# Performance work log

Measured on AMD Instinct MI355X. Metric: run time of the kernel, lower is better.

The kernel has to match this reference:

```python
import jax, jax.numpy as jnp
import numpy as np

EPS = 1e-5


def _gcn_conv(x, src, dst, norm, W, b, n_nodes):
    # PyG GCNConv: transform, then normalized scatter-add aggregation (self-loops included in src/dst)
    h = x @ W                                   # [N, out]
    msg = h[src] * norm[:, None]                # gather over edges [E+N, out]
    agg = jax.ops.segment_sum(msg, dst, num_segments=n_nodes)
    return agg + b


def _bn(x, gamma, beta):
    # BatchNorm1d in training mode: batch stats over node axis, biased variance
    mu = jnp.mean(x, axis=0)
    var = jnp.mean((x - mu) ** 2, axis=0)
    return (x - mu) * jax.lax.rsqrt(var + EPS) * gamma + beta


def setup_inputs() -> dict:
    key = jax.random.key(0)
    ks = jax.random.split(key, 8)
    N, E, F_in, H, F_out = 50000, 800000, 32, 96, 2
    x = jax.random.normal(ks[0], (N, F_in), dtype=jnp.float32)
    edge_index = jax.random.randint(ks[1], (2, E), 0, N, dtype=jnp.int64)
    def lin(k, fi, fo):
        s = 1.0 / np.sqrt(fi)
        return jax.random.uniform(k, (fi, fo), jnp.float32, -s, s)
    W1 = lin(ks[2], F_in, H); b1 = jnp.zeros((H,), jnp.float32)
    W2 = lin(ks[3], H, H);    b2 = jnp.zeros((H,), jnp.float32)
    W3 = lin(ks[4], H, H);    b3 = jnp.zeros((H,), jnp.float32)
    W4 = lin(ks[5], H, F_out); b4 = jnp.zeros((F_out,), jnp.float32)
    g1 = jnp.ones((H,), jnp.float32); be1 = jnp.zeros((H,), jnp.float32)
    g2 = jnp.ones((H,), jnp.float32); be2 = jnp.zeros((H,), jnp.float32)
    g3 = jnp.ones((H,), jnp.float32); be3 = jnp.zeros((H,), jnp.float32)
    return dict(x=x, edge_index=edge_index,
                W1=W1, b1=b1, g1=g1, be1=be1,
                W2=W2, b2=b2, g2=g2, be2=be2,
                W3=W3, b3=b3, g3=g3, be3=be3,
                W4=W4, b4=b4)


def reference(x, edge_index, W1, b1, g1, be1, W2, b2, g2, be2, W3, b3, g3, be3, W4, b4):
    N = x.shape[0]
    loop = jnp.arange(N, dtype=edge_index.dtype)
    src = jnp.concatenate([edge_index[0], loop])   # add self-loops
    dst = jnp.concatenate([edge_index[1], loop])
    deg = jax.ops.segment_sum(jnp.ones_like(dst, dtype=x.dtype), dst, num_segments=N)
    dinv = jnp.where(deg > 0, jax.lax.rsqrt(deg), 0.0)
    norm = dinv[src] * dinv[dst]                   # D^{-1/2} (A+I) D^{-1/2}

    h = jax.nn.relu(_bn(_gcn_conv(x, src, dst, norm, W1, b1, N), g1, be1))
    h = jax.nn.relu(_bn(_gcn_conv(h, src, dst, norm, W2, b2, N), g2, be2))
    h = jax.nn.relu(_bn(_gcn_conv(h, src, dst, norm, W3, b3, N), g3, be3))
    return _gcn_conv(h, src, dst, norm, W4, b4, N)
```

## Files before the change

kernel.cpp:

```cpp
#include <hip/hip_runtime.h>
#include <hip/hip_bf16.h>

using bf16x8 = __attribute__((ext_vector_type(8))) short;
using f32x4  = __attribute__((ext_vector_type(4))) float;

#define FS_CHUNK 4096

__device__ __forceinline__ float ldf(const void* p, size_t i, float isf){
  if (isf > 0.5f) return ((const float*)p)[i];
  unsigned int u = ((unsigned int)((const unsigned short*)p)[i]) << 16;
  return __uint_as_float(u);
}
__device__ __forceinline__ unsigned short f2bf(float v){
  unsigned int u = __float_as_uint(v);
  u = (u + 0x7FFFu + ((u >> 16) & 1u)) >> 16;
  return (unsigned short)u;
}
__device__ __forceinline__ unsigned int pk2(float a, float b){
  return (unsigned int)f2bf(a) | ((unsigned int)f2bf(b) << 16);
}
__device__ __forceinline__ float lo16(unsigned int u){ return __uint_as_float(u << 16); }
__device__ __forceinline__ float hi16(unsigned int u){ return __uint_as_float(u & 0xFFFF0000u); }

__global__ void k_fill(unsigned short* o, unsigned short v, int n){
  int i = blockIdx.x*blockDim.x + threadIdx.x;
  if (i < n) o[i] = v;
}

__global__ void k_prep(const unsigned short* xh, const unsigned int* eu,
                       float* flag, int nelemX, long long E,
                       const void* W1, const void* W2, const void* W3, const void* W4,
                       unsigned short* __restrict__ Wt1, unsigned short* __restrict__ Wt2,
                       unsigned short* __restrict__ Wt3, float* __restrict__ W4f,
                       int* __restrict__ cnt, float* __restrict__ stAll, int n){
  int t = threadIdx.x;
  if (blockIdx.x > 0){
    int total = n + 4609;
    for (int i = (int)(blockIdx.x-1)*256 + t; i < total; i += (int)(gridDim.x-1)*256){
      if (i < n) cnt[i] = 0; else stAll[i - n] = 0.f;
    }
    return;
  }
  __shared__ int sf32, si64;
  __shared__ float sisf;
  if (t == 0){ sf32 = 0; si64 = 1; }
  __syncthreads();
  {
    int i = 2*t;
    if (i < nelemX){
      unsigned e8 = (xh[i] >> 7) & 0xFFu;
      if (e8 >= 140u) sf32 = 1;
    }
    if ((long long)(2*t + 1) < 2*E){
      if (eu[2*t + 1] != 0u) si64 = 0;
    }
  }
  __syncthreads();
  if (t == 0){
    flag[0] = (float)sf32; flag[1] = (float)si64;
    sisf = (float)sf32;
  }
  __syncthreads();
  float isf = sisf;
  for (int q = t; q < 3072; q += 256){
    int nn = q >> 5, k = q & 31;
    Wt1[q] = f2bf(ldf(W1, (size_t)96*k + nn, isf));
  }
  for (int q = t; q < 9216; q += 256){
    int nn = q/96, k = q - 96*nn;
    Wt2[q] = f2bf(ldf(W2, (size_t)96*k + nn, isf));
    Wt3[q] = f2bf(ldf(W3, (size_t)96*k + nn, isf));
  }
  if (t < 192) W4f[t] = ldf(W4, t, isf);
}

__global__ void k_cnt2(const int* __restrict__ ei, const float* __restrict__ flag,
                       int* __restrict__ cnt, int* __restrict__ ec,
                       long long E, int n){
  long long i = (long long)blockIdx.x*blockDim.x + threadIdx.x;
  long long i0 = 2*i;
  if (i0 >= E) return;
  bool i64 = (flag[1] > 0.5f);
  bool two = (i0 + 1 < E);
  int s0, d0, s1 = 0, d1 = -1;
  if ((E & 1LL) == 0){
    if (i64){
      uint4 vs = ((const uint4*)ei)[i];
      uint4 vd = ((const uint4*)(ei + 2*E))[i];
      s0 = (int)vs.x; s1 = (int)vs.z; d0 = (int)vd.x; d1 = (int)vd.z;
    } else {
      int2 vs = ((const int2*)ei)[i];
      int2 vd = ((const int2*)(ei + E))[i];
      s0 = vs.x; s1 = vs.y; d0 = vd.x; d1 = vd.y;
    }
  } else {
    if (i64){ s0 = ei[2*i0]; d0 = ei[2*E + 2*i0];
              if (two){ s1 = ei[2*i0+2]; d1 = ei[2*E + 2*i0 + 2]; } }
    else    { s0 = ei[i0];   d0 = ei[E + i0];
              if (two){ s1 = ei[i0+1];   d1 = ei[E + i0 + 1]; } }
  }
  bool ok0 = ((unsigned)s0 < (unsigned)n) && ((unsigned)d0 < (unsigned)n);
  bool ok1 = two && ((unsigned)s1 < (unsigned)n) && ((unsigned)d1 < (unsigned)n);
  if (!ok0){ s0 = -1; d0 = -1; }
  if (!ok1){ s1 = -1; d1 = -1; }
  if (two){
    int4 o; o.x = s0; o.y = d0; o.z = s1; o.w = d1;
    ((int4*)ec)[i] = o;
  } else {
    int2 o; o.x = s0; o.y = d0;
    ((int2*)ec)[i0] = o;
  }
  if (ok0) atomicAdd(&cnt[d0], 1);
  if (ok1) atomicAdd(&cnt[d1], 1);
}

__global__ void k_emit2(const int* __restrict__ cnt, int* __restrict__ gctr,
                        int* __restrict__ rowst, int* __restrict__ cursor,
                        float* __restrict__ dinv, int n){
  int i = blockIdx.x*256 + threadIdx.x;
  int lane = threadIdx.x & 63;
  int v = (i < n) ? cnt[i] : 0;
  int s = v;
  #pragma unroll
  for (int off = 1; off < 64; off <<= 1){
    int u = __shfl_up(s, off, 64);
    if (lane >= off) s += u;
  }
  int wtot = __shfl(s, 63, 64);
  int base = 0;
  if (lane == 63) base = atomicAdd(gctr, wtot);
  base = __shfl(base, 63, 64);
  if (i < n){
    int r = base + s - v;
    rowst[i]  = r;
    cursor[i] = r;
    dinv[i]   = rsqrtf((float)(1 + v));
  }
}

template<typename IT>
__global__ __launch_bounds__(256) void k_fx(const int* __restrict__ ec,
      int* __restrict__ cursor, IT* __restrict__ csr,
      long long E, int n, int gF8,
      const void* __restrict__ x, const float* __restrict__ flag,
      const float* __restrict__ dinv, unsigned short* __restrict__ XS){
  int t = threadIdx.x;
  if ((int)blockIdx.x < gF8){
    int part = blockIdx.x & 7;
    long long base = (long long)(blockIdx.x >> 3) * FS_CHUNK;
    int pl = (int)(((long long)n *  part     ) >> 3);
    int pr = (int)(((long long)n * (part + 1)) >> 3);
    long long lim = base + FS_CHUNK < E ? base + FS_CHUNK : E;
    for (long long i = base + 2*t; i < lim; i += 512){
      int4 v = ((const int4*)ec)[i >> 1];
      if (v.y >= pl && v.y < pr && (unsigned)v.x < (unsigned)n){
        int p = atomicAdd(&cursor[v.y], 1);
        csr[p] = (IT)v.x;
      }
      if (i + 1 < lim && v.w >= pl && v.w < pr && (unsigned)v.z < (unsigned)n){
        int p = atomicAdd(&cursor[v.w], 1);
        csr[p] = (IT)v.z;
      }
    }
    return;
  }
  int q = (int)(blockIdx.x - gF8)*256 + t;
  if (q < 4*n){
    int node = q >> 2, part = q & 3;
    float isf = flag[0];
    float di = dinv[node];
    uint4 o;
    if (isf > 0.5f){
      const float* xr = (const float*)x + (size_t)32*node + 8*part;
      o.x = pk2(xr[0]*di, xr[1]*di); o.y = pk2(xr[2]*di, xr[3]*di);
      o.z = pk2(xr[4]*di, xr[5]*di); o.w = pk2(xr[6]*di, xr[7]*di);
    } else {
      uint4 v = ((const uint4*)x)[(size_t)4*node + part];
      o.x = pk2(lo16(v.x)*di, hi16(v.x)*di);
      o.y = pk2(lo16(v.y)*di, hi16(v.y)*di);
      o.z = pk2(lo16(v.z)*di, hi16(v.z)*di);
      o.w = pk2(lo16(v.w)*di, hi16(v.w)*di);
    }
    ((uint4*)XS)[q] = o;
  }
}

#define ACC8(v) { a0+=lo16((v).x); a1+=hi16((v).x); a2+=lo16((v).y); a3+=hi16((v).y); \
                  a4+=lo16((v).z); a5+=hi16((v).z); a6+=lo16((v).w); a7+=hi16((v).w); }

template<typename IT>
__global__ __launch_bounds__(256) void k_aggx(const uint4* __restrict__ xs4,
      const int* __restrict__ rowst, const int* __restrict__ cnt,
      const IT* __restrict__ csr, const float* __restrict__ dinv,
      const unsigned short* __restrict__ Wt1b,
      unsigned short* __restrict__ Zb, float* __restrict__ stout, int n){
  __shared__ __align__(16) unsigned short Xs[64][40];
  __shared__ __align__(16) unsigned short Wt[96][40];
  __shared__ float bs[96], bq[96];
  int t = threadIdx.x;
  for (int q = t; q < 384; q += 256){
    uint4 v = ((const uint4*)Wt1b)[q];
    *(uint4*)&Wt[q >> 2][(q & 3)*8] = v;
  }
  if (t < 96){ bs[t] = 0.f; bq[t] = 0.f; }
  int g = t & 3, ty = t >> 2;
  int node = blockIdx.x*64 + ty;
  float a0=0.f,a1=0.f,a2=0.f,a3=0.f,a4=0.f,a5=0.f,a6=0.f,a7=0.f;
  if (node < n){
    uint4 v = xs4[(size_t)node*4 + g];
    ACC8(v);
    int b = rowst[node], e = b + cnt[node];
    int j = b;
    for (; j + 7 < e; j += 8){
      uint4 v0 = xs4[(size_t)csr[j]  *4 + g];
      uint4 v1 = xs4[(size_t)csr[j+1]*4 + g];
      uint4 v2 = xs4[(size_t)csr[j+2]*4 + g];
      uint4 v3 = xs4[(size_t)csr[j+3]*4 + g];
      uint4 v4 = xs4[(size_t)csr[j+4]*4 + g];
      uint4 v5 = xs4[(size_t)csr[j+5]*4 + g];
      uint4 v6 = xs4[(size_t)csr[j+6]*4 + g];
      uint4 v7 = xs4[(size_t)csr[j+7]*4 + g];
      ACC8(v0); ACC8(v1); ACC8(v2); ACC8(v3);
      ACC8(v4); ACC8(v5); ACC8(v6); ACC8(v7);
    }
    for (; j + 3 < e; j += 4){
      uint4 v0 = xs4[(size_t)csr[j]  *4 + g];
      uint4 v1 = xs4[(size_t)csr[j+1]*4 + g];
      uint4 v2 = xs4[(size_t)csr[j+2]*4 + g];
      uint4 v3 = xs4[(size_t)csr[j+3]*4 + g];
      ACC8(v0); ACC8(v1); ACC8(v2); ACC8(v3);
    }
    for (; j < e; ++j){
      uint4 vv = xs4[(size_t)csr[j]*4 + g];
      ACC8(vv);
    }
    float di = dinv[node];
    a0*=di; a1*=di; a2*=di; a3*=di; a4*=di; a5*=di; a6*=di; a7*=di;
  }
  uint4 o;
  o.x = pk2(a0,a1); o.y = pk2(a2,a3); o.z = pk2(a4,a5); o.w = pk2(a6,a7);
  *(uint4*)&Xs[ty][8*g] = o;
  __syncthreads();
  int wv = t >> 6, lane = t & 63;
  int m = lane & 15, quad = lane >> 4;
  bf16x8 av = *(const bf16x8*)&Xs[16*wv + m][8*quad];
  f32x4 acc[6];
  #pragma unroll
  for (int c = 0; c < 6; ++c) acc[c] = (f32x4)(0.f);
  #pragma unroll
  for (int c = 0; c < 6; ++c){
    bf16x8 bv = *(const bf16x8*)&Wt[16*c + m][8*quad];
    acc[c] = __builtin_amdgcn_mfma_f32_16x16x32_bf16(av, bv, acc[c], 0, 0, 0);
  }
  int rowbase = blockIdx.x*64 + 16*wv + 4*quad;
  #pragma unroll
  for (int c = 0; c < 6; ++c){
    int col = 16*c + m;
    float s = 0.f, q = 0.f;
    #pragma unroll
    for (int r = 0; r < 4; ++r){
      int rr = rowbase + r;
      if (rr < n){
        unsigned short h = f2bf(acc[c][r]);
        Zb[(size_t)96*rr + col] = h;
        float br = __uint_as_float(((unsigned int)h) << 16);
        s += br; q += br*br;
      }
    }
    atomicAdd(&bs[col], s);
    atomicAdd(&bq[col], q);
  }
  __syncthreads();
  if (t < 96){
    int rep = blockIdx.x & 7;
    atomicAdd(&stout[192*rep + t],      bs[t]);
    atomicAdd(&stout[192*rep + 96 + t], bq[t]);
  }
}

template<typename IT>
__global__ __launch_bounds__(192) void k_agg(const uint4* __restrict__ hsr,
      const int* __restrict__ rowst, const int* __restrict__ cnt,
      const IT* __restrict__ csr,
      const float* __restrict__ dinv, uint4* __restrict__ zb4,
      float* __restrict__ stout, int n){
  __shared__ float ls[16][97], lq[16][97];
  int g = threadIdx.x, ty = threadIdx.y;
  int t = ty*12 + g;
  int node = blockIdx.x*16 + ty;
  float r[8];
  if (node < n){
    uint4 v = hsr[(size_t)node*12 + g];
    float a0 = lo16(v.x), a1 = hi16(v.x), a2 = lo16(v.y), a3 = hi16(v.y);
    float a4 = lo16(v.z), a5 = hi16(v.z), a6 = lo16(v.w), a7 = hi16(v.w);
    int b = rowst[node], e = b + cnt[node];
    int j = b;
    for (; j + 7 < e; j += 8){
      uint4 v0 = hsr[(size_t)csr[j]  *12 + g];
      uint4 v1 = hsr[(size_t)csr[j+1]*12 + g];
      uint4 v2 = hsr[(size_t)csr[j+2]*12 + g];
      uint4 v3 = hsr[(size_t)csr[j+3]*12 + g];
      uint4 v4 = hsr[(size_t)csr[j+4]*12 + g];
      uint4 v5 = hsr[(size_t)csr[j+5]*12 + g];
      uint4 v6 = hsr[(size_t)csr[j+6]*12 + g];
      uint4 v7 = hsr[(size_t)csr[j+7]*12 + g];
      ACC8(v0); ACC8(v1); ACC8(v2); ACC8(v3);
      ACC8(v4); ACC8(v5); ACC8(v6); ACC8(v7);
    }
    for (; j + 3 < e; j += 4){
      uint4 v0 = hsr[(size_t)csr[j]  *12 + g];
      uint4 v1 = hsr[(size_t)csr[j+1]*12 + g];
      uint4 v2 = hsr[(size_t)csr[j+2]*12 + g];
      uint4 v3 = hsr[(size_t)csr[j+3]*12 + g];
      ACC8(v0); ACC8(v1); ACC8(v2); ACC8(v3);
    }
    for (; j < e; ++j){
      uint4 vv = hsr[(size_t)csr[j]*12 + g];
      ACC8(vv);
    }
    float di = dinv[node];
    uint4 o;
    o.x = pk2(a0*di, a1*di);
    o.y = pk2(a2*di, a3*di);
    o.z = pk2(a4*di, a5*di);
    o.w = pk2(a6*di, a7*di);
    zb4[(size_t)node*12 + g] = o;
    r[0]=lo16(o.x); r[1]=hi16(o.x); r[2]=lo16(o.y); r[3]=hi16(o.y);
    r[4]=lo16(o.z); r[5]=hi16(o.z); r[6]=lo16(o.w); r[7]=hi16(o.w);
  } else {
    #pragma unroll
    for (int jj = 0; jj < 8; ++jj) r[jj] = 0.f;
  }
  #pragma unroll
  for (int jj = 0; jj < 8; ++jj){
    ls[ty][8*g + jj] = r[jj];
    lq[ty][8*g + jj] = r[jj]*r[jj];
  }
  __syncthreads();
  if (t < 96){
    float s = 0.f, q = 0.f;
    #pragma unroll
    for (int rr = 0; rr < 16; ++rr){ s += ls[rr][t]; q += lq[rr][t]; }
    int rep = blockIdx.x & 7;
    atomicAdd(&stout[192*rep + t],      s);
    atomicAdd(&stout[192*rep + 96 + t], q);
  }
}

__global__ __launch_bounds__(256) void k_linm(const unsigned short* __restrict__ zb,
      const unsigned short* __restrict__ Wtb, const float* __restrict__ st,
      const void* __restrict__ gam, const void* __restrict__ bet,
      const float* __restrict__ flag, const float* __restrict__ dinv,
      unsigned short* __restrict__ HS, int n, float invN){
  __shared__ float sa[96], sc[96];
  __shared__ __align__(16) unsigned short Ys[64][104];
  __shared__ __align__(16) unsigned short Wt[96][104];
  int t = threadIdx.x;
  if (t < 96){
    float ssum = 0.f, qsum = 0.f;
    #pragma unroll
    for (int r = 0; r < 8; ++r){ ssum += st[192*r + t]; qsum += st[192*r + 96 + t]; }
    float isf = flag[0];
    float mu  = ssum*invN;
    float var = fmaxf(qsum*invN - mu*mu, 0.f);
    float istd = rsqrtf(var + 1e-5f);
    float a = ldf(gam, t, isf)*istd;
    sa[t] = a; sc[t] = ldf(bet, t, isf) - mu*a;
  }
  for (int q = t; q < 1152; q += 256){
    uint4 v = ((const uint4*)Wtb)[q];
    *(uint4*)&Wt[q/12][8*(q - 12*(q/12))] = v;
  }
  __syncthreads();
  {
    int row = t >> 2, part = t & 3;
    int node = blockIdx.x*64 + row;
    if (node < n){
      const uint4* zr = (const uint4*)(zb + (size_t)96*node) + 3*part;
      #pragma unroll
      for (int q = 0; q < 3; ++q){
        uint4 zz = zr[q];
        int k = 24*part + 8*q;
        float y0 = fmaxf(lo16(zz.x)*sa[k]   + sc[k],   0.f);
        float y1 = fmaxf(hi16(zz.x)*sa[k+1] + sc[k+1], 0.f);
        float y2 = fmaxf(lo16(zz.y)*sa[k+2] + sc[k+2], 0.f);
        float y3 = fmaxf(hi16(zz.y)*sa[k+3] + sc[k+3], 0.f);
        float y4 = fmaxf(lo16(zz.z)*sa[k+4] + sc[k+4], 0.f);
        float y5 = fmaxf(hi16(zz.z)*sa[k+5] + sc[k+5], 0.f);
        float y6 = fmaxf(lo16(zz.w)*sa[k+6] + sc[k+6], 0.f);
        float y7 = fmaxf(hi16(zz.w)*sa[k+7] + sc[k+7], 0.f);
        *(unsigned int*)&Ys[row][k]     = pk2(y0, y1);
        *(unsigned int*)&Ys[row][k + 2] = pk2(y2, y3);
        *(unsigned int*)&Ys[row][k + 4] = pk2(y4, y5);
        *(unsigned int*)&Ys[row][k + 6] = pk2(y6, y7);
      }
    } else {
      unsigned int* yp = (unsigned int*)&Ys[row][24*part];
      #pragma unroll
      for (int q = 0; q < 12; ++q) yp[q] = 0u;
    }
  }
  __syncthreads();
  int wv = t >> 6, lane = t & 63;
  int m = lane & 15, quad = lane >> 4;
  bf16x8 av[3];
  #pragma unroll
  for (int kt = 0; kt < 3; ++kt)
    av[kt] = *(const bf16x8*)&Ys[16*wv + m][32*kt + 8*quad];
  f32x4 acc[6];
  #pragma unroll
  for (int c = 0; c < 6; ++c) acc[c] = (f32x4)(0.f);
  #pragma unroll
  for (int c = 0; c < 6; ++c){
    const unsigned short* wrow = &Wt[16*c + m][8*quad];
    #pragma unroll
    for (int kt = 0; kt < 3; ++kt){
      bf16x8 bv = *(const bf16x8*)(wrow + 32*kt);
      acc[c] = __builtin_amdgcn_mfma_f32_16x16x32_bf16(av[kt], bv, acc[c], 0, 0, 0);
    }
  }
  int rowbase = blockIdx.x*64 + 16*wv + 4*quad;
  float div[4];
  #pragma unroll
  for (int r = 0; r < 4; ++r){ int rr = rowbase + r; div[r] = (rr < n) ? dinv[rr] : 0.f; }
  #pragma unroll
  for (int c = 0; c < 6; ++c){
    int col = 16*c + m;
    #pragma unroll
    for (int r = 0; r < 4; ++r){
      int rr = rowbase + r;
      if (rr < n) HS[(size_t)96*rr + col] = f2bf(acc[c][r]*div[r]);
    }
  }
}

__global__ __launch_bounds__(256) void k_lin4(const unsigned short* __restrict__ zb,
      const float* __restrict__ Wf, const float* __restrict__ st,
      const void* __restrict__ gam, const void* __restrict__ bet,
      const float* __restrict__ flag, const float* __restrict__ dinv,
      float* __restrict__ hs2, int n, float invN){
  __shared__ float sa[96], sc[96];
  int t = threadIdx.x;
  if (t < 96){
    float ssum = 0.f, qsum = 0.f;
    #pragma unroll
    for (int r = 0; r < 8; ++r){ ssum += st[192*r + t]; qsum += st[192*r + 96 + t]; }
    float isf = flag[0];
    float mu  = ssum*invN;
    float var = fmaxf(qsum*invN - mu*mu, 0.f);
    float istd = rsqrtf(var + 1e-5f);
    float a = ldf(gam, t, isf)*istd;
    sa[t] = a; sc[t] = ldf(bet, t, isf) - mu*a;
  }
  __syncthreads();
  int i = blockIdx.x*blockDim.x + t;
  if (i >= n) return;
  const uint4* zr = (const uint4*)(zb + (size_t)96*i);
  float a0 = 0.f, a1 = 0.f;
  #pragma unroll
  for (int q = 0; q < 12; ++q){
    uint4 zz = zr[q];
    int k = 8*q;
    float y;
    y = fmaxf(lo16(zz.x)*sa[k]   + sc[k],   0.f); a0 += y*Wf[2*k];    a1 += y*Wf[2*k+1];
    y = fmaxf(hi16(zz.x)*sa[k+1] + sc[k+1], 0.f); a0 += y*Wf[2*k+2];  a1 += y*Wf[2*k+3];
    y = fmaxf(lo16(zz.y)*sa[k+2] + sc[k+2], 0.f); a0 += y*Wf[2*k+4];  a1 += y*Wf[2*k+5];
    y = fmaxf(hi16(zz.y)*sa[k+3] + sc[k+3], 0.f); a0 += y*Wf[2*k+6];  a1 += y*Wf[2*k+7];
    y = fmaxf(lo16(zz.z)*sa[k+4] + sc[k+4], 0.f); a0 += y*Wf[2*k+8];  a1 += y*Wf[2*k+9];
    y = fmaxf(hi16(zz.z)*sa[k+5] + sc[k+5], 0.f); a0 += y*Wf[2*k+10]; a1 += y*Wf[2*k+11];
    y = fmaxf(lo16(zz.w)*sa[k+6] + sc[k+6], 0.f); a0 += y*Wf[2*k+12]; a1 += y*Wf[2*k+13];
    y = fmaxf(hi16(zz.w)*sa[k+7] + sc[k+7], 0.f); a0 += y*Wf[2*k+14]; a1 += y*Wf[2*k+15];
  }
  float di = dinv[i];
  hs2[(size_t)2*i]   = di*a0;
  hs2[(size_t)2*i+1] = di*a1;
}

template<typename IT>
__global__ void k_agg2(const float2* __restrict__ hs2, const int* __restrict__ rowst,
                       const int* __restrict__ cnt, const IT* __restrict__ csr,
                       const float* __restrict__ dinv,
                       const void* __restrict__ b4, const float* __restrict__ flag,
                       void* __restrict__ out, int n){
  int node = blockIdx.x*blockDim.x + threadIdx.x;
  if (node >= n) return;
  float2 a = hs2[node];
  int b = rowst[node], e = b + cnt[node];
  int j = b;
  for (; j + 3 < e; j += 4){
    float2 v0 = hs2[(size_t)csr[j]];
    float2 v1 = hs2[(size_t)csr[j+1]];
    float2 v2 = hs2[(size_t)csr[j+2]];
    float2 v3 = hs2[(size_t)csr[j+3]];
    a.x += v0.x + v1.x + v2.x + v3.x;
    a.y += v0.y + v1.y + v2.y + v3.y;
  }
  for (; j < e; ++j){
    float2 v = hs2[(size_t)csr[j]];
    a.x += v.x; a.y += v.y;
  }
  float isf = flag[0];
  float di = dinv[node];
  float v0 = a.x*di + ldf(b4, 0, isf);
  float v1 = a.y*di + ldf(b4, 1, isf);
  if (isf > 0.5f){
    ((float*)out)[(size_t)2*node]   = v0;
    ((float*)out)[(size_t)2*node+1] = v1;
  } else {
    ((unsigned short*)out)[(size_t)2*node]   = f2bf(v0);
    ((unsigned short*)out)[(size_t)2*node+1] = f2bf(v1);
  }
}

extern "C" void kernel_launch(void* const* d_in, const int* in_sizes, int n_in,
                              void* d_out, int out_size, void* d_ws, size_t ws_size,
                              hipStream_t stream)
{
  const int B = 256;
  unsigned short* outh = (unsigned short*)d_out;

  if (n_in < 16){
    k_fill<<<(out_size+B-1)/B, B, 0, stream>>>(outh, 0x3F40u, out_size); return;
  }
  const int N = in_sizes[0] / 32;
  const long long E = in_sizes[1] / 2;
  if (in_sizes[0] % 32 != 0 || out_size != 2*N){
    k_fill<<<(out_size+B-1)/B, B, 0, stream>>>(outh, 0x3F60u, out_size); return;
  }
  const bool u16 = (N < 65536);

  size_t Npad = ((size_t)N + 3) & ~(size_t)3;
  float* ws   = (float*)d_ws;
  float* dinv = ws;
  float* hs2  = dinv + Npad;
  float* flag = hs2 + (size_t)2*N;
  float* stAll= flag + 4;
  float* W4f  = stAll + 4612;
  unsigned short* Wt1b = (unsigned short*)(W4f + 192);
  unsigned short* Wt2b = Wt1b + 3072;
  unsigned short* Wt3b = Wt2b + 9216;
  int* cnt    = (int*)(Wt3b + 9216);
  int* cursor = cnt + N;
  int* rowst  = cursor + N;
  void* csrv  = (void*)(rowst + N);
  size_t csrBytes = (size_t)E * (u16 ? 2 : 4);
  uintptr_t hp_ = (uintptr_t)csrv + csrBytes;
  hp_ = (hp_ + 15) & ~(uintptr_t)15;
  unsigned short* HS = (unsigned short*)hp_;
  unsigned short* Zb = HS + (size_t)96*N;
  int* ec = (int*)(Zb + (size_t)96*N);

  size_t needB = ((uintptr_t)(ec + 2*E + 4) - (uintptr_t)d_ws) + 64;
  if (ws_size < needB){
    k_fill<<<(out_size+B-1)/B, B, 0, stream>>>(outh, 0x3F00u, out_size); return;
  }

  unsigned short* XS = HS;

  const void* x  = d_in[0];
  const int*  ei = (const int*)d_in[1];
  const void* W1 = d_in[2];
  const void* g1 = d_in[4];  const void* be1 = d_in[5];
  const void* W2 = d_in[6];
  const void* g2 = d_in[8];  const void* be2 = d_in[9];
  const void* W3 = d_in[10];
  const void* g3 = d_in[12]; const void* be3 = d_in[13];
  const void* W4 = d_in[14];
  const void* b4 = d_in[15];

  float* stA = stAll;
  float* stB = stAll + 1536;
  float* stC = stAll + 3072;
  int*   gctr = (int*)(stAll + 4608);

  int gN  = (N + B - 1)/B;
  long long hE = (E + 1)/2;
  int gE2 = (int)((hE + B - 1)/B); if (gE2 < 1) gE2 = 1;
  int nb  = (N + 255)/256;
  int gA  = (N + 15)/16;
  int gL  = (N + 63)/64;
  int gXS = (4*N + 255)/256;
  int gF8 = (int)((E + FS_CHUNK - 1)/FS_CHUNK) * 8;
  float invN = 1.0f / (float)N;
  dim3 ablk(12,16);

  k_prep<<<33, B, 0, stream>>>((const unsigned short*)x, (const unsigned int*)ei,
                               flag, in_sizes[0], E, W1, W2, W3, W4,
                               Wt1b, Wt2b, Wt3b, W4f, cnt, stAll, N);
  k_cnt2<<<gE2, B, 0, stream>>>(ei, flag, cnt, ec, E, N);
  k_emit2<<<nb, B, 0, stream>>>(cnt, gctr, rowst, cursor, dinv, N);

  if (u16){
    unsigned short* csr = (unsigned short*)csrv;
    k_fx<unsigned short><<<gF8 + gXS, B, 0, stream>>>(ec, cursor, csr, E, N, gF8,
                                                      x, flag, dinv, XS);
    k_aggx<unsigned short><<<gL, B, 0, stream>>>((const uint4*)XS, rowst, cnt, csr, dinv, Wt1b, Zb, stA, N);
    k_linm<<<gL, B, 0, stream>>>(Zb, Wt2b, stA, g1, be1, flag, dinv, HS, N, invN);
    k_agg<unsigned short><<<gA, ablk, 0, stream>>>((const uint4*)HS, rowst, cnt, csr, dinv, (uint4*)Zb, stB, N);
    k_linm<<<gL, B, 0, stream>>>(Zb, Wt3b, stB, g2, be2, flag, dinv, HS, N, invN);
    k_agg<unsigned short><<<gA, ablk, 0, stream>>>((const uint4*)HS, rowst, cnt, csr, dinv, (uint4*)Zb, stC, N);
    k_lin4<<<gN, B, 0, stream>>>(Zb, W4f, stC, g3, be3, flag, dinv, hs2, N, invN);
    k_agg2<unsigned short><<<gN, B, 0, stream>>>((const float2*)hs2, rowst, cnt, csr, dinv, b4, flag, d_out, N);
  } else {
    int* csr = (int*)csrv;
    k_fx<int><<<gF8 + gXS, B, 0, stream>>>(ec, cursor, csr, E, N, gF8,
                                           x, flag, dinv, XS);
    k_aggx<int><<<gL, B, 0, stream>>>((const uint4*)XS, rowst, cnt, csr, dinv, Wt1b, Zb, stA, N);
    k_linm<<<gL, B, 0, stream>>>(Zb, Wt2b, stA, g1, be1, flag, dinv, HS, N, invN);
    k_agg<int><<<gA, ablk, 0, stream>>>((const uint4*)HS, rowst, cnt, csr, dinv, (uint4*)Zb, stB, N);
    k_linm<<<gL, B, 0, stream>>>(Zb, Wt3b, stB, g2, be2, flag, dinv, HS, N, invN);
    k_agg<int><<<gA, ablk, 0, stream>>>((const uint4*)HS, rowst, cnt, csr, dinv, (uint4*)Zb, stC, N);
    k_lin4<<<gN, B, 0, stream>>>(Zb, W4f, stC, g3, be3, flag, dinv, hs2, N, invN);
    k_agg2<int><<<gN, B, 0, stream>>>((const float2*)hs2, rowst, cnt, csr, dinv, b4, flag, d_out, N);
  }
}
```

Before: 329.9 us.

## Fuse full GCN pipeline into one persistent cooperative kernel with grid syncs

Replaces the sequence of about ten separate kernel launches (prep, count, scan, CSR fill, four aggregate and linear stages) with a single cooperative persistent kernel that loops over tiles and separates phases with grid.sync(). The aim is to remove per-launch overhead and the idle gaps between dependent small kernels. In exchange, occupancy is capped at 256 CUs times 4 blocks and every phase must use grid-stride loops. The grid barriers also add cost, and some phases such as the aggregation tile of 21 nodes may map work less efficiently than the tuned standalone kernels. The old multi-kernel path remains as a fallback if the cooperative launch fails.

Result: slower. 936.3 us (+183.8%).

```diff
diff --git a/kernel.cpp b/kernel.cpp
--- a/kernel.cpp
+++ b/kernel.cpp
@@ -1,5 +1,8 @@
 #include <hip/hip_runtime.h>
 #include <hip/hip_bf16.h>
+#include <hip/hip_cooperative_groups.h>
+
+namespace cg = cooperative_groups;
 
 using bf16x8 = __attribute__((ext_vector_type(8))) short;
 using f32x4  = __attribute__((ext_vector_type(4))) float;
@@ -26,6 +29,40 @@
   int i = blockIdx.x*blockDim.x + threadIdx.x;
   if (i < n) o[i] = v;
 }
+
+struct WSL {
+  float *dinv, *hs2, *flag, *stAll, *W4f;
+  unsigned short *Wt1b, *Wt2b, *Wt3b;
+  int *cnt, *cursor, *rowst;
+  unsigned short *HS, *Zb;
+  int *ec, *gctr;
+};
+template<typename IT>
+__host__ __device__ inline void mkws(char* base, int n, long long E, WSL& w, IT*& csr){
+  size_t Npad = ((size_t)n + 3) & ~(size_t)3;
+  float* ws = (float*)base;
+  w.dinv = ws;
+  w.hs2  = w.dinv + Npad;
+  w.flag = w.hs2 + (size_t)2*n;
+  w.stAll= w.flag + 4;
+  w.W4f  = w.stAll + 4612;
+  w.Wt1b = (unsigned short*)(w.W4f + 192);
+  w.Wt2b = w.Wt1b + 3072;
+  w.Wt3b = w.Wt2b + 9216;
+  w.cnt  = (int*)(w.Wt3b + 9216);
+  w.cursor = w.cnt + n;
+  w.rowst  = w.cursor + n;
+  csr = (IT*)(w.rowst + n);
+  uintptr_t hp = (uintptr_t)(csr + E);
+  hp = (hp + 15) & ~(uintptr_t)15;
+  w.HS = (unsigned short*)hp;
+  w.Zb = w.HS + (size_t)96*n;
+  w.ec = (int*)(w.Zb + (size_t)96*n);
+  w.gctr = (int*)(w.stAll + 4608);
+}
+
+#define ACC8(v) { a0+=lo16((v).x); a1+=hi16((v).x); a2+=lo16((v).y); a3+=hi16((v).y); \
+                  a4+=lo16((v).z); a5+=hi16((v).z); a6+=lo16((v).w); a7+=hi16((v).w); }
 
 __global__ void k_prep(const unsigned short* xh, const unsigned int* eu,
                        float* flag, int nelemX, long long E,
@@ -184,9 +221,6 @@
     ((uint4*)XS)[q] = o;
   }
 }
-
-#define ACC8(v) { a0+=lo16((v).x); a1+=hi16((v).x); a2+=lo16((v).y); a3+=hi16((v).y); \
-                  a4+=lo16((v).z); a5+=hi16((v).z); a6+=lo16((v).w); a7+=hi16((v).w); }
 
 template<typename IT>
 __global__ __launch_bounds__(256) void k_aggx(const uint4* __restrict__ xs4,
@@ -512,6 +546,523 @@
   }
 }
 
+
+__device__ __forceinline__ void phase_linm_d(unsigned char* SM,
+    const unsigned short* zb, const unsigned short* Wtb, const float* st,
+    const void* gam, const void* bet, float isf, const float* dinv,
+    unsigned short* HS, int n, float invN, int b, int G, int t)
+{
+  float* sa = (float*)SM;
+  float* sc = (float*)(SM + 384);
+  typedef unsigned short RowY[104];
+  RowY* Ys = (RowY*)(SM + 768);
+  RowY* Wt = (RowY*)(SM + 768 + 13312);
+  if (t < 96){
+    float ssum = 0.f, qsum = 0.f;
+    #pragma unroll
+    for (int r = 0; r < 8; ++r){ ssum += st[192*r + t]; qsum += st[192*r + 96 + t]; }
+    float mu  = ssum*invN;
+    float var = fmaxf(qsum*invN - mu*mu, 0.f);
+    float istd = rsqrtf(var + 1e-5f);
+    float a = ldf(gam, t, isf)*istd;
+    sa[t] = a; sc[t] = ldf(bet, t, isf) - mu*a;
+  }
+  for (int q = t; q < 1152; q += 256){
+    uint4 v = ((const uint4*)Wtb)[q];
+    int rr = q/12;
+    *(uint4*)&Wt[rr][8*(q - 12*rr)] = v;
+  }
+  int wv = t >> 6, lane = t & 63;
+  int m = lane & 15, quad = lane >> 4;
+  int row = t >> 2, part = t & 3;
+  int gT = (n + 63) >> 6;
+  for (int tile = b; tile < gT; tile += G){
+    __syncthreads();
+    int node = tile*64 + row;
+    if (node < n){
+      const uint4* zr = (const uint4*)(zb + (size_t)96*node) + 3*part;
+      #pragma unroll
+      for (int q = 0; q < 3; ++q){
+        uint4 zz = zr[q];
+        int k = 24*part + 8*q;
+        float y0 = fmaxf(lo16(zz.x)*sa[k]   + sc[k],   0.f);
+        float y1 = fmaxf(hi16(zz.x)*sa[k+1] + sc[k+1], 0.f);
+        float y2 = fmaxf(lo16(zz.y)*sa[k+2] + sc[k+2], 0.f);
+        float y3 = fmaxf(hi16(zz.y)*sa[k+3] + sc[k+3], 0.f);
+        float y4 = fmaxf(lo16(zz.z)*sa[k+4] + sc[k+4], 0.f);
+        float y5 = fmaxf(hi16(zz.z)*sa[k+5] + sc[k+5], 0.f);
+        float y6 = fmaxf(lo16(zz.w)*sa[k+6] + sc[k+6], 0.f);
+        float y7 = fmaxf(hi16(zz.w)*sa[k+7] + sc[k+7], 0.f);
+        *(unsigned int*)&Ys[row][k]     = pk2(y0, y1);
+        *(unsigned int*)&Ys[row][k + 2] = pk2(y2, y3);
+        *(unsigned int*)&Ys[row][k + 4] = pk2(y4, y5);
+        *(unsigned int*)&Ys[row][k + 6] = pk2(y6, y7);
+      }
+    } else {
+      unsigned int* yp = (unsigned int*)&Ys[row][24*part];
+      #pragma unroll
+      for (int q = 0; q < 12; ++q) yp[q] = 0u;
+    }
+    __syncthreads();
+    bf16x8 av[3];
+    #pragma unroll
+    for (int kt = 0; kt < 3; ++kt)
+      av[kt] = *(const bf16x8*)&Ys[16*wv + m][32*kt + 8*quad];
+    f32x4 acc[6];
+    #pragma unroll
+    for (int c = 0; c < 6; ++c) acc[c] = (f32x4)(0.f);
+    #pragma unroll
+    for (int c = 0; c < 6; ++c){
+      const unsigned short* wrow = &Wt[16*c + m][8*quad];
+      #pragma unroll
+      for (int kt = 0; kt < 3; ++kt){
+        bf16x8 bv = *(const bf16x8*)(wrow + 32*kt);
+        acc[c] = __builtin_amdgcn_mfma_f32_16x16x32_bf16(av[kt], bv, acc[c], 0, 0, 0);
+      }
+    }
+    int rowbase = tile*64 + 16*wv + 4*quad;
+    float dv[4];
+    #pragma unroll
+    for (int r = 0; r < 4; ++r){ int rr = rowbase + r; dv[r] = (rr < n) ? dinv[rr] : 0.f; }
+    #pragma unroll
+    for (int c = 0; c < 6; ++c){
+      int col = 16*c + m;
+      #pragma unroll
+      for (int r = 0; r < 4; ++r){
+        int rr = rowbase + r;
+        if (rr < n) HS[(size_t)96*rr + col] = f2bf(acc[c][r]*dv[r]);
+      }
+    }
+  }
+}
+
+template<typename IT>
+__device__ __forceinline__ void phase_agg_d(unsigned char* SM, const uint4* hsr,
+    const int* rowst, const int* cnt, const IT* csr, const float* dinv,
+    uint4* zb4, float* stout, int n, int b, int G, int t)
+{
+  typedef float Row97[97];
+  Row97* ls = (Row97*)SM;
+  Row97* lq = (Row97*)(SM + 8148);
+  int ty = t / 12, g = t - 12*ty;
+  int gT = (n + 20) / 21;
+  for (int tile = b; tile < gT; tile += G){
+    float r[8];
+    #pragma unroll
+    for (int jj = 0; jj < 8; ++jj) r[jj] = 0.f;
+    int node = tile*21 + ty;
+    if (ty < 21 && node < n){
+      uint4 v = hsr[(size_t)node*12 + g];
+      float a0 = lo16(v.x), a1 = hi16(v.x), a2 = lo16(v.y), a3 = hi16(v.y);
+      float a4 = lo16(v.z), a5 = hi16(v.z), a6 = lo16(v.w), a7 = hi16(v.w);
+      int bb = rowst[node], e = bb + cnt[node];
+      int j = bb;
+      for (; j + 7 < e; j += 8){
+        uint4 v0 = hsr[(size_t)csr[j]  *12 + g];
+        uint4 v1 = hsr[(size_t)csr[j+1]*12 + g];
+        uint4 v2 = hsr[(size_t)csr[j+2]*12 + g];
+        uint4 v3 = hsr[(size_t)csr[j+3]*12 + g];
+        uint4 v4 = hsr[(size_t)csr[j+4]*12 + g];
+        uint4 v5 = hsr[(size_t)csr[j+5]*12 + g];
+        uint4 v6 = hsr[(size_t)csr[j+6]*12 + g];
+        uint4 v7 = hsr[(size_t)csr[j+7]*12 + g];
+        ACC8(v0); ACC8(v1); ACC8(v2); ACC8(v3);
+        ACC8(v4); ACC8(v5); ACC8(v6); ACC8(v7);
+      }
+      for (; j + 3 < e; j += 4){
+        uint4 v0 = hsr[(size_t)csr[j]  *12 + g];
+        uint4 v1 = hsr[(size_t)csr[j+1]*12 + g];
+        uint4 v2 = hsr[(size_t)csr[j+2]*12 + g];
+        uint4 v3 = hsr[(size_t)csr[j+3]*12 + g];
+        ACC8(v0); ACC8(v1); ACC8(v2); ACC8(v3);
+      }
+      for (; j < e; ++j){
+        uint4 vv = hsr[(size_t)csr[j]*12 + g];
+        ACC8(vv);
+      }
+      float di = dinv[node];
+      uint4 o;
+      o.x = pk2(a0*di, a1*di);
+      o.y = pk2(a2*di, a3*di);
+      o.z = pk2(a4*di, a5*di);
+      o.w = pk2(a6*di, a7*di);
+      zb4[(size_t)node*12 + g] = o;
+      r[0]=lo16(o.x); r[1]=hi16(o.x); r[2]=lo16(o.y); r[3]=hi16(o.y);
+      r[4]=lo16(o.z); r[5]=hi16(o.z); r[6]=lo16(o.w); r[7]=hi16(o.w);
+    }
+    if (ty < 21){
+      #pragma unroll
+      for (int jj = 0; jj < 8; ++jj){
+        ls[ty][8*g + jj] = r[jj];
+        lq[ty][8*g + jj] = r[jj]*r[jj];
+      }
+    }
+    __syncthreads();
+    if (t < 96){
+      float s = 0.f, q = 0.f;
+      #pragma unroll
+      for (int rr = 0; rr < 21; ++rr){ s += ls[rr][t]; q += lq[rr][t]; }
+      int rep = tile & 7;
+      atomicAdd(&stout[192*rep + t],      s);
+      atomicAdd(&stout[192*rep + 96 + t], q);
+    }
+    __syncthreads();
+  }
+}
+
+template<typename IT>
+__global__ __launch_bounds__(256, 4) void k_main(
+    char* wsBase, const void* x, const int* ei,
+    const void* W1, const void* W2, const void* W3, const void* W4,
+    const void* g1, const void* be1, const void* g2, const void* be2,
+    const void* g3, const void* be3, const void* b4,
+    void* outp, int nelemX, long long E, int n, float invN)
+{
+  cg::grid_group grid = cg::this_grid();
+  WSL w; IT* csr;
+  mkws<IT>(wsBase, n, E, w, csr);
+  const int t = threadIdx.x;
+  const int G = (int)gridDim.x;
+  const int b = (int)blockIdx.x;
+  __shared__ __align__(16) unsigned char SM[34048];
+  __shared__ int sdet[2];
+
+  if (b < 3){
+    const unsigned short* xh = (const unsigned short*)x;
+    const unsigned int* eu = (const unsigned int*)ei;
+    if (t == 0){ sdet[0] = 0; sdet[1] = 1; }
+    __syncthreads();
+    {
+      int i = 2*t;
+      if (i < nelemX){
+        unsigned e8 = (xh[i] >> 7) & 0xFFu;
+        if (e8 >= 140u) sdet[0] = 1;
+      }
+      if ((long long)(2*t + 1) < 2*E){
+        if (eu[2*t + 1] != 0u) sdet[1] = 0;
+      }
+    }
+    __syncthreads();
+    float isf = (float)sdet[0];
+    if (b == 0){
+      if (t == 0){ w.flag[0] = isf; w.flag[1] = (float)sdet[1]; }
+      for (int q = t; q < 3072; q += 256){
+        int nn = q >> 5, k = q & 31;
+        w.Wt1b[q] = f2bf(ldf(W1, (size_t)96*k + nn, isf));
+      }
+      if (t < 192) w.W4f[t] = ldf(W4, t, isf);
+    } else if (b == 1){
+      for (int q = t; q < 9216; q += 256){
+        int nn = q/96, k = q - 96*nn;
+        w.Wt2b[q] = f2bf(ldf(W2, (size_t)96*k + nn, isf));
+      }
+    } else {
+      for (int q = t; q < 9216; q += 256){
+        int nn = q/96, k = q - 96*nn;
+        w.Wt3b[q] = f2bf(ldf(W3, (size_t)96*k + nn, isf));
+      }
+    }
+  } else {
+    int total = n + 4609;
+    for (int i = (b-3)*256 + t; i < total; i += (G-3)*256){
+      if (i < n) w.cnt[i] = 0; else w.stAll[i - n] = 0.f;
+    }
+  }
+  grid.sync();
+
+  const bool  i64f = (w.flag[1] > 0.5f);
+  const float isfG = w.flag[0];
+
+  {
+    long long hE = (E + 1) >> 1;
+    long long stride = (long long)G * 256;
+    bool evenE = ((E & 1LL) == 0);
+    for (long long ii = (long long)b*256 + t; ii < hE; ii += stride){
+      long long i0 = 2*ii;
+      bool two = (i0 + 1 < E);
+      int s0, d0, s1 = 0, d1 = -1;
+      if (evenE){
+        if (i64f){
+          uint4 vs = ((const uint4*)ei)[ii];
+          uint4 vd = ((const uint4*)(ei + 2*E))[ii];
+          s0 = (int)vs.x; s1 = (int)vs.z; d0 = (int)vd.x; d1 = (int)vd.z;
+        } else {
+          int2 vs = ((const int2*)ei)[ii];
+          int2 vd = ((const int2*)(ei + E))[ii];
+          s0 = vs.x; s1 = vs.y; d0 = vd.x; d1 = vd.y;
+        }
+      } else {
+        if (i64f){ s0 = ei[2*i0]; d0 = ei[2*E + 2*i0];
+                   if (two){ s1 = ei[2*i0+2]; d1 = ei[2*E + 2*i0 + 2]; } }
+        else    { s0 = ei[i0];   d0 = ei[E + i0];
+                   if (two){ s1 = ei[i0+1];   d1 = ei[E + i0 + 1]; } }
+      }
+      bool ok0 = ((unsigned)s0 < (unsigned)n) && ((unsigned)d0 < (unsigned)n);
+      bool ok1 = two && ((unsigned)s1 < (unsigned)n) && ((unsigned)d1 < (unsigned)n);
+      if (!ok0){ s0 = -1; d0 = -1; }
+      if (!ok1){ s1 = -1; d1 = -1; }
+      if (two){
+        int4 o; o.x = s0; o.y = d0; o.z = s1; o.w = d1;
+        ((int4*)w.ec)[ii] = o;
+      } else {
+        int2 o; o.x = s0; o.y = d0;
+        ((int2*)w.ec)[i0] = o;
+      }
+      if (ok0) atomicAdd(&w.cnt[d0], 1);
+      if (ok1) atomicAdd(&w.cnt[d1], 1);
+    }
+  }
+  grid.sync();
+
+  {
+    int lane = t & 63;
+    int nRound = (n + 255) & ~255;
+    for (int base0 = b*256; base0 < nRound; base0 += G*256){
+      int i = base0 + t;
+      int v = (i < n) ? w.cnt[i] : 0;
+      int s = v;
+      #pragma unroll
+      for (int off = 1; off < 64; off <<= 1){
+        int u = __shfl_up(s, off, 64);
+        if (lane >= off) s += u;
+      }
+      int wtot = __shfl(s, 63, 64);
+      int base = 0;
+      if (lane == 63) base = atomicAdd(w.gctr, wtot);
+      base = __shfl(base, 63, 64);
+      if (i < n){
+        int r = base + s - v;
+        w.rowst[i]  = r;
+        w.cursor[i] = r;
+        w.dinv[i]   = rsqrtf((float)(1 + v));
+      }
+    }
+  }
+  grid.sync();
+
+  {
+    long long nChunks = (E + FS_CHUNK - 1) / FS_CHUNK;
+    int FB = ((G*3)/4) & ~7;
+    if (FB < 8) FB = 8;
+    if (FB > G - 8) FB = (G - 8) & ~7;
+    if (b < FB){
+      int part = b & 7;
+      int pl = (int)(((long long)n *  part     ) >> 3);
+      int pr = (int)(((long long)n * (part + 1)) >> 3);
+      for (long long c = b >> 3; c < nChunks; c += (long long)(FB >> 3)){
+        long long base = c * FS_CHUNK;
+        long long lim = base + FS_CHUNK < E ? base + FS_CHUNK : E;
+        for (long long i = base + 2*t; i < lim; i += 512){
+          int4 v = ((const int4*)w.ec)[i >> 1];
+          if (v.y >= pl && v.y < pr && (unsigned)v.x < (unsigned)n){
+            int p = atomicAdd(&w.cursor[v.y], 1);
+            csr[p] = (IT)v.x;
+          }
+          if (i + 1 < lim && v.w >= pl && v.w < pr && (unsigned)v.z < (unsigned)n){
+            int p = atomicAdd(&w.cursor[v.w], 1);
+            csr[p] = (IT)v.z;
+          }
+        }
+      }
+    } else {
+      unsigned short* XS = w.HS;
+      for (int q = (b - FB)*256 + t; q < 4*n; q += (G - FB)*256){
+        int node = q >> 2, part = q & 3;
+        float di = w.dinv[node];
+        uint4 o;
+        if (isfG > 0.5f){
+          const float* xr = (const float*)x + (size_t)32*node + 8*part;
+          o.x = pk2(xr[0]*di, xr[1]*di); o.y = pk2(xr[2]*di, xr[3]*di);
+          o.z = pk2(xr[4]*di, xr[5]*di); o.w = pk2(xr[6]*di, xr[7]*di);
+        } else {
+          uint4 v = ((const uint4*)x)[(size_t)4*node + part];
+          o.x = pk2(lo16(v.x)*di, hi16(v.x)*di);
+          o.y = pk2(lo16(v.y)*di, hi16(v.y)*di);
+          o.z = pk2(lo16(v.z)*di, hi16(v.z)*di);
+          o.w = pk2(lo16(v.w)*di, hi16(v.w)*di);
+        }
+        ((uint4*)XS)[q] = o;
+      }
+    }
+  }
+  grid.sync();
+
+  {
+    typedef unsigned short Row40[40];
+    Row40* Xs = (Row40*)SM;
+    Row40* Wt = (Row40*)(SM + 5120);
+    float* bs = (float*)(SM + 12800);
+    float* bq = (float*)(SM + 13184);
+    const uint4* xs4 = (const uint4*)w.HS;
+    for (int q = t; q < 384; q += 256){
+      uint4 v = ((const uint4*)w.Wt1b)[q];
+      *(uint4*)&Wt[q >> 2][(q & 3)*8] = v;
+    }
+    int g = t & 3, ty = t >> 2;
+    int wv = t >> 6, lane = t & 63;
+    int m = lane & 15, quad = lane >> 4;
+    int gT = (n + 63) >> 6;
+    float* stA = w.stAll;
+    for (int tile = b; tile < gT; tile += G){
+      __syncthreads();
+      if (t < 96){ bs[t] = 0.f; bq[t] = 0.f; }
+      int node = tile*64 + ty;
+      float a0=0.f,a1=0.f,a2=0.f,a3=0.f,a4=0.f,a5=0.f,a6=0.f,a7=0.f;
+      if (node < n){
+        uint4 v = xs4[(size_t)node*4 + g];
+        ACC8(v);
+        int bb = w.rowst[node], e = bb + w.cnt[node];
+        int j = bb;
+        for (; j + 7 < e; j += 8){
+          uint4 v0 = xs4[(size_t)csr[j]  *4 + g];
+          uint4 v1 = xs4[(size_t)csr[j+1]*4 + g];
+          uint4 v2 = xs4[(size_t)csr[j+2]*4 + g];
+          uint4 v3 = xs4[(size_t)csr[j+3]*4 + g];
+          uint4 v4 = xs4[(size_t)csr[j+4]*4 + g];
+          uint4 v5 = xs4[(size_t)csr[j+5]*4 + g];
+          uint4 v6 = xs4[(size_t)csr[j+6]*4 + g];
+          uint4 v7 = xs4[(size_t)csr[j+7]*4 + g];
+          ACC8(v0); ACC8(v1); ACC8(v2); ACC8(v3);
+          ACC8(v4); ACC8(v5); ACC8(v6); ACC8(v7);
+        }
+        for (; j + 3 < e; j += 4){
+          uint4 v0 = xs4[(size_t)csr[j]  *4 + g];
+          uint4 v1 = xs4[(size_t)csr[j+1]*4 + g];
+          uint4 v2 = xs4[(size_t)csr[j+2]*4 + g];
+          uint4 v3 = xs4[(size_t)csr[j+3]*4 + g];
+          ACC8(v0); ACC8(v1); ACC8(v2); ACC8(v3);
+        }
+        for (; j < e; ++j){
+          uint4 vv = xs4[(size_t)csr[j]*4 + g];
+          ACC8(vv);
+        }
+        float di = w.dinv[node];
+        a0*=di; a1*=di; a2*=di; a3*=di; a4*=di; a5*=di; a6*=di; a7*=di;
+      }
+      uint4 o;
+      o.x = pk2(a0,a1); o.y = pk2(a2,a3); o.z = pk2(a4,a5); o.w = pk2(a6,a7);
+      *(uint4*)&Xs[ty][8*g] = o;
+      __syncthreads();
+      bf16x8 av = *(const bf16x8*)&Xs[16*wv + m][8*quad];
+      f32x4 acc[6];
+      #pragma unroll
+      for (int c = 0; c < 6; ++c) acc[c] = (f32x4)(0.f);
+      #pragma unroll
+      for (int c = 0; c < 6; ++c){
+        bf16x8 bv = *(const bf16x8*)&Wt[16*c + m][8*quad];
+        acc[c] = __builtin_amdgcn_mfma_f32_16x16x32_bf16(av, bv, acc[c], 0, 0, 0);
+      }
+      int rowbase = tile*64 + 16*wv + 4*quad;
+      #pragma unroll
+      for (int c = 0; c < 6; ++c){
+        int col = 16*c + m;
+        float s = 0.f, q = 0.f;
+        #pragma unroll
+        for (int r = 0; r < 4; ++r){
+          int rr = rowbase + r;
+          if (rr < n){
+            unsigned short h = f2bf(acc[c][r]);
+            w.Zb[(size_t)96*rr + col] = h;
+            float br = __uint_as_float(((unsigned int)h) << 16);
+            s += br; q += br*br;
+          }
+        }
+        atomicAdd(&bs[col], s);
+        atomicAdd(&bq[col], q);
+      }
+      __syncthreads();
+      if (t < 96){
+        int rep = tile & 7;
+        atomicAdd(&stA[192*rep + t],      bs[t]);
+        atomicAdd(&stA[192*rep + 96 + t], bq[t]);
+      }
+    }
+  }
+  grid.sync();
+
+  phase_linm_d(SM, w.Zb, w.Wt2b, w.stAll, g1, be1, isfG, w.dinv, w.HS, n, invN, b, G, t);
+  grid.sync();
+  phase_agg_d<IT>(SM, (const uint4*)w.HS, w.rowst, w.cnt, csr, w.dinv,
+                  (uint4*)w.Zb, w.stAll + 1536, n, b, G, t);
+  grid.sync();
+  phase_linm_d(SM, w.Zb, w.Wt3b, w.stAll + 1536, g2, be2, isfG, w.dinv, w.HS, n, invN, b, G, t);
+  grid.sync();
+  phase_agg_d<IT>(SM, (const uint4*)w.HS, w.rowst, w.cnt, csr, w.dinv,
+                  (uint4*)w.Zb, w.stAll + 3072, n, b, G, t);
+  grid.sync();
+
+  {
+    float* sa = (float*)SM;
+    float* sc = (float*)(SM + 384);
+    const float* st = w.stAll + 3072;
+    if (t < 96){
+      float ssum = 0.f, qsum = 0.f;
+      #pragma unroll
+      for (int r = 0; r < 8; ++r){ ssum += st[192*r + t]; qsum += st[192*r + 96 + t]; }
+      float mu  = ssum*invN;
+      float var = fmaxf(qsum*invN - mu*mu, 0.f);
+      float istd = rsqrtf(var + 1e-5f);
+      float a = ldf(g3, t, isfG)*istd;
+      sa[t] = a; sc[t] = ldf(be3, t, isfG) - mu*a;
+    }
+    __syncthreads();
+    const float* Wf = w.W4f;
+    for (int i = b*256 + t; i < n; i += G*256){
+      const uint4* zr = (const uint4*)(w.Zb + (size_t)96*i);
+      float a0 = 0.f, a1 = 0.f;
+      #pragma unroll
+      for (int q = 0; q < 12; ++q){
+        uint4 zz = zr[q];
+        int k = 8*q;
+        float y;
+        y = fmaxf(lo16(zz.x)*sa[k]   + sc[k],   0.f); a0 += y*Wf[2*k];    a1 += y*Wf[2*k+1];
+        y = fmaxf(hi16(zz.x)*sa[k+1] + sc[k+1], 0.f); a0 += y*Wf[2*k+2];  a1 += y*Wf[2*k+3];
+        y = fmaxf(lo16(zz.y)*sa[k+2] + sc[k+2], 0.f); a0 += y*Wf[2*k+4];  a1 += y*Wf[2*k+5];
+        y = fmaxf(hi16(zz.y)*sa[k+3] + sc[k+3], 0.f); a0 += y*Wf[2*k+6];  a1 += y*Wf[2*k+7];
+        y = fmaxf(lo16(zz.z)*sa[k+4] + sc[k+4], 0.f); a0 += y*Wf[2*k+8];  a1 += y*Wf[2*k+9];
+        y = fmaxf(hi16(zz.z)*sa[k+5] + sc[k+5], 0.f); a0 += y*Wf[2*k+10]; a1 += y*Wf[2*k+11];
+        y = fmaxf(lo16(zz.w)*sa[k+6] + sc[k+6], 0.f); a0 += y*Wf[2*k+12]; a1 += y*Wf[2*k+13];
+        y = fmaxf(hi16(zz.w)*sa[k+7] + sc[k+7], 0.f); a0 += y*Wf[2*k+14]; a1 += y*Wf[2*k+15];
+      }
+      float di = w.dinv[i];
+      w.hs2[(size_t)2*i]   = di*a0;
+      w.hs2[(size_t)2*i+1] = di*a1;
+    }
+  }
+  grid.sync();
+
+  {
+    const float2* h2 = (const float2*)w.hs2;
+    for (int node = b*256 + t; node < n; node += G*256){
+      float2 a = h2[node];
+      int bb = w.rowst[node], e = bb + w.cnt[node];
+      int j = bb;
+      for (; j + 3 < e; j += 4){
+        float2 v0 = h2[(size_t)csr[j]];
+        float2 v1 = h2[(size_t)csr[j+1]];
+        float2 v2 = h2[(size_t)csr[j+2]];
+        float2 v3 = h2[(size_t)csr[j+3]];
+        a.x += v0.x + v1.x + v2.x + v3.x;
+        a.y += v0.y + v1.y + v2.y + v3.y;
+      }
+      for (; j < e; ++j){
+        float2 v = h2[(size_t)csr[j]];
+        a.x += v.x; a.y += v.y;
+      }
+      float di = w.dinv[node];
+      float v0 = a.x*di + ldf(b4, 0, isfG);
+      float v1 = a.y*di + ldf(b4, 1, isfG);
+      if (isfG > 0.5f){
+        ((float*)outp)[(size_t)2*node]   = v0;
+        ((float*)outp)[(size_t)2*node+1] = v1;
+      } else {
+        ((unsigned short*)outp)[(size_t)2*node]   = f2bf(v0);
+        ((unsigned short*)outp)[(size_t)2*node+1] = f2bf(v1);
+      }
+    }
+  }
+}
+
 extern "C" void kernel_launch(void* const* d_in, const int* in_sizes, int n_in,
                               void* d_out, int out_size, void* d_ws, size_t ws_size,
                               hipStream_t stream)
@@ -529,33 +1080,21 @@
   }
   const bool u16 = (N < 65536);
 
-  size_t Npad = ((size_t)N + 3) & ~(size_t)3;
-  float* ws   = (float*)d_ws;
-  float* dinv = ws;
-  float* hs2  = dinv + Npad;
-  float* flag = hs2 + (size_t)2*N;
-  float* stAll= flag + 4;
-  float* W4f  = stAll + 4612;
-  unsigned short* Wt1b = (unsigned short*)(W4f + 192);
-  unsigned short* Wt2b = Wt1b + 3072;
-  unsigned short* Wt3b = Wt2b + 9216;
-  int* cnt    = (int*)(Wt3b + 9216);
-  int* cursor = cnt + N;
-  int* rowst  = cursor + N;
-  void* csrv  = (void*)(rowst + N);
-  size_t csrBytes = (size_t)E * (u16 ? 2 : 4);
-  uintptr_t hp_ = (uintptr_t)csrv + csrBytes;
-  hp_ = (hp_ + 15) & ~(uintptr_t)15;
-  unsigned short* HS = (unsigned short*)hp_;
-  unsigned short* Zb = HS + (size_t)96*N;
-  int* ec = (int*)(Zb + (size_t)96*N);
-
-  size_t needB = ((uintptr_t)(ec + 2*E + 4) - (uintptr_t)d_ws) + 64;
+  WSL w;
+  char* wsB = (char*)d_ws;
+  size_t needB;
+  if (u16){
+    unsigned short* csr_;
+    mkws<unsigned short>(wsB, N, E, w, csr_);
+    needB = ((uintptr_t)(w.ec + 2*E + 4) - (uintptr_t)d_ws) + 64;
+  } else {
+    int* csr_;
+    mkws<int>(wsB, N, E, w, csr_);
+    needB = ((uintptr_t)(w.ec + 2*E + 4) - (uintptr_t)d_ws) + 64;
+  }
   if (ws_size < needB){
     k_fill<<<(out_size+B-1)/B, B, 0, stream>>>(outh, 0x3F00u, out_size); return;
   }
-
-  unsigned short* XS = HS;
 
   const void* x  = d_in[0];
   const int*  ei = (const int*)d_in[1];
@@ -568,20 +1107,63 @@
   const void* W4 = d_in[14];
   const void* b4 = d_in[15];
 
+  float invN = 1.0f / (float)N;
+  int nelemX = in_sizes[0];
+  long long Ell = E;
+  int Nn = N;
+  void* outp = d_out;
+
+  {
+    static int mb_u16 = -1, mb_i32 = -1;
+    int& mb = u16 ? mb_u16 : mb_i32;
+    if (mb < 0){
+      int v = 0;
+      hipError_t e = hipOccupancyMaxActiveBlocksPerMultiprocessor(&v,
+          u16 ? (const void*)k_main<unsigned short> : (const void*)k_main<int>,
+          256, 0);
+      if (e != hipSuccess) v = 0;
+      mb = v;
+    }
+    if (mb >= 1){
+      int blkPerCU = mb < 4 ? mb : 4;
+      int grid = 256 * blkPerCU;
+      if (grid >= 64){
+        void* kargs[] = {
+          (void*)&wsB, (void*)&x, (void*)&ei,
+          (void*)&W1, (void*)&W2, (void*)&W3, (void*)&W4,
+          (void*)&g1, (void*)&be1, (void*)&g2, (void*)&be2,
+          (void*)&g3, (void*)&be3, (void*)&b4,
+          (void*)&outp, (void*)&nelemX, (void*)&Ell, (void*)&Nn, (void*)&invN
+        };
+        hipError_t le = hipLaunchCooperativeKernel(
+            u16 ? (const void*)k_main<unsigned short> : (const void*)k_main<int>,
+            dim3(grid), dim3(256), kargs, 0, stream);
+        if (le == hipSuccess) return;
+      }
+    }
+  }
+
+  float* dinv = w.dinv; float* hs2 = w.hs2; float* flag = w.flag;
+  float* stAll = w.stAll; float* W4f = w.W4f;
+  unsigned short* Wt1b = w.Wt1b; unsigned short* Wt2b = w.Wt2b; unsigned short* Wt3b = w.Wt3b;
+  int* cnt = w.cnt; int* cursor = w.cursor; int* rowst = w.rowst;
+  unsigned short* HS = w.HS; unsigned short* Zb = w.Zb;
+  int* ec = w.ec;
+  void* csrv = (void*)(rowst + N);
+
   float* stA = stAll;
   float* stB = stAll + 1536;
   float* stC = stAll + 3072;
-  int*   gctr = (int*)(stAll + 4608);
+  int*   gctr = w.gctr;
 
   int gN  = (N + B - 1)/B;
-  long long hE = (E + 1)/2;
-  int gE2 = (int)((hE + B - 1)/B); if (gE2 < 1) gE2 = 1;
+  long long hEp = (E + 1)/2;
+  int gE2 = (int)((hEp + B - 1)/B); if (gE2 < 1) gE2 = 1;
   int nb  = (N + 255)/256;
   int gA  = (N + 15)/16;
   int gL  = (N + 63)/64;
   int gXS = (4*N + 255)/256;
   int gF8 = (int)((E + FS_CHUNK - 1)/FS_CHUNK) * 8;
-  float invN = 1.0f / (float)N;
   dim3 ablk(12,16);
 
   k_prep<<<33, B, 0, stream>>>((const unsigned short*)x, (const unsigned int*)ei,
@@ -590,6 +1172,7 @@
   k_cnt2<<<gE2, B, 0, stream>>>(ei, flag, cnt, ec, E, N);
   k_emit2<<<nb, B, 0, stream>>>(cnt, gctr, rowst, cursor, dinv, N);
 
+  unsigned short* XS = HS;
   if (u16){
     unsigned short* csr = (unsigned short*)csrv;
     k_fx<unsigned short><<<gF8 + gXS, B, 0, stream>>>(ec, cursor, csr, E, N, gF8,
```
